# Performance work log

Measured on AMD Instinct MI355X. Metric: run time of the kernel, lower is better.

Reference implementation:

```python
import jax, jax.numpy as jnp
import numpy as np

EPS = 1e-5

def _ln(x, g, b):
    mu = jnp.mean(x, axis=-1, keepdims=True)
    var = jnp.var(x, axis=-1, keepdims=True)
    return (x - mu) * jax.lax.rsqrt(var + EPS) * g + b

def setup_inputs() -> dict:
    key = jax.random.key(0)
    ks = jax.random.split(key, 12)
    B, N, D, C = 1, 512, 128, 128
    s = 0.02
    return {
        "Z_raw": jax.random.normal(ks[0], (B, N, N, D), jnp.float32),
        "Z_mask_row": jnp.ones((B, N, N), jnp.float32),
        "ln1_g": jnp.ones((D,), jnp.float32),
        "ln1_b": jnp.zeros((D,), jnp.float32),
        "W_lr": jax.random.normal(ks[1], (D, 2 * C), jnp.float32) * s,
        "b_lr": jnp.zeros((2 * C,), jnp.float32),
        "W_gate": jax.random.normal(ks[2], (D, 2 * C), jnp.float32) * s,
        "b_gate": jnp.ones((2 * C,), jnp.float32),
        "W_og": jax.random.normal(ks[3], (D, D), jnp.float32) * s,
        "b_og": jnp.ones((D,), jnp.float32),
        "ln2_g": jnp.ones((C,), jnp.float32),
        "ln2_b": jnp.zeros((C,), jnp.float32),
        "W_op": jax.random.normal(ks[4], (C, D), jnp.float32) * s,
        "out_bias": jnp.zeros((D,), jnp.float32),
    }

def reference(Z_raw, Z_mask_row, ln1_g, ln1_b, W_lr, b_lr, W_gate, b_gate,
              W_og, b_og, ln2_g, ln2_b, W_op, out_bias):
    # Z_raw: [B,N,N,D]; Z_mask_row: [B,N,N]
    Z = _ln(Z_raw, ln1_g, ln1_b)
    lr = (Z @ W_lr + b_lr) * Z_mask_row[..., None]           # [B,N,N,2C]
    lr = lr * jax.nn.sigmoid(Z @ W_gate + b_gate)
    C = lr.shape[-1] // 2
    left, right = lr[..., :C], lr[..., C:]                    # [B,N,N,C]
    g = jax.nn.sigmoid(Z @ W_og + b_og)                       # [B,N,N,D]
    # triangle outgoing: p[b,i,j,c] = sum_k left[b,i,k,c] * right[b,j,k,c]
    p = jnp.einsum('bikc,bjkc->bijc', left, right)
    ab = _ln(p, ln2_g, ln2_b) @ W_op                          # [B,N,N,D]
    # eval mode: dropout mask is ones -> plain gated bias + residual
    return Z_raw + g * (ab + out_bias)
```

## Files before the change

kernel.cpp:

```cpp
#include <hip/hip_runtime.h>
#include <hip/hip_bf16.h>

#define NSEQ 512
#define DDIM 128
#define NPOS (NSEQ*NSEQ)

typedef __bf16 bf16x8 __attribute__((ext_vector_type(8)));
typedef float f32x4 __attribute__((ext_vector_type(4)));
typedef unsigned short us4 __attribute__((ext_vector_type(4)));
typedef unsigned int u32x4 __attribute__((ext_vector_type(4)));

__device__ __forceinline__ unsigned short f2bf(float f){
  unsigned int u = __float_as_uint(f);
  u += 0x7fffu + ((u >> 16) & 1u);
  return (unsigned short)(u >> 16);
}
__device__ __forceinline__ float bf2f(unsigned short s){
  return __uint_as_float(((unsigned int)s) << 16);
}
__device__ __forceinline__ float sigmoidf_(float x){
  return 1.0f/(1.0f + __expf(-x));
}

__global__ void k_prep(const float* __restrict__ Wlr, const float* __restrict__ Wgate,
                       const float* __restrict__ Wog, const float* __restrict__ Wop,
                       unsigned short* __restrict__ wt)
{
  int idx = blockIdx.x*256 + threadIdx.x;
  if (idx >= 768*128) return;
  int row = idx >> 7, k = idx & 127;
  float v;
  if (row < 256)      v = Wlr[k*256 + row];
  else if (row < 512) v = Wgate[k*256 + (row-256)];
  else if (row < 640) v = Wog[k*128 + (row-512)];
  else                v = Wop[k*128 + (row-640)];
  wt[idx] = f2bf(v);
}

__device__ __forceinline__ void mfma_k128(const unsigned short (&A)[128][136],
                                          const unsigned short (&B)[128][136],
                                          int wrow, int wcol, int lr_, int lq,
                                          f32x4 (&acc)[4][4])
{
  #pragma unroll
  for (int s = 0; s < 4; ++s){
    const int k0 = s*32 + lq*8;
    bf16x8 a[4], b[4];
    #pragma unroll
    for (int f = 0; f < 4; ++f)
      a[f] = *reinterpret_cast<const bf16x8*>(&A[wrow*64 + f*16 + lr_][k0]);
    #pragma unroll
    for (int f = 0; f < 4; ++f)
      b[f] = *reinterpret_cast<const bf16x8*>(&B[wcol*64 + f*16 + lr_][k0]);
    #pragma unroll
    for (int fi = 0; fi < 4; ++fi)
      #pragma unroll
      for (int fj = 0; fj < 4; ++fj)
        acc[fi][fj] = __builtin_amdgcn_mfma_f32_16x16x32_bf16(a[fi], b[fj], acc[fi][fj], 0, 0, 0);
  }
}

__global__ __launch_bounds__(256, 2)
void k1(const float* __restrict__ Zraw, const float* __restrict__ mask,
        const float* __restrict__ ln1g, const float* __restrict__ ln1b,
        const float* __restrict__ blr, const float* __restrict__ bgate,
        const float* __restrict__ bog,
        const unsigned short* __restrict__ wt,
        unsigned short* __restrict__ left_t, unsigned short* __restrict__ right_t,
        unsigned short* __restrict__ g_ws)
{
  __shared__ unsigned short zln[128][136];
  __shared__ unsigned short wchunk[128][136];

  const int t = threadIdx.x;
  const int posb = blockIdx.x * 128;
  const int r = t >> 1, h = t & 1;

  {
    const float* src = Zraw + (size_t)(posb + r)*DDIM + h*64;
    float v[64];
    float s = 0.f, sq = 0.f;
    #pragma unroll
    for (int i = 0; i < 16; ++i){
      f32x4 x = *reinterpret_cast<const f32x4*>(src + i*4);
      v[i*4+0] = x[0]; v[i*4+1] = x[1]; v[i*4+2] = x[2]; v[i*4+3] = x[3];
    }
    #pragma unroll
    for (int i = 0; i < 64; ++i){ s += v[i]; sq += v[i]*v[i]; }
    s  += __shfl_xor(s, 1);
    sq += __shfl_xor(sq, 1);
    float mu = s * (1.0f/128.0f);
    float var = sq * (1.0f/128.0f) - mu*mu;
    float rs = rsqrtf(var + 1e-5f);
    #pragma unroll
    for (int i = 0; i < 32; ++i){
      int c0 = h*64 + 2*i;
      float a = (v[2*i]   - mu)*rs*ln1g[c0]   + ln1b[c0];
      float b = (v[2*i+1] - mu)*rs*ln1g[c0+1] + ln1b[c0+1];
      *reinterpret_cast<unsigned int*>(&zln[r][c0]) =
          (unsigned int)f2bf(a) | ((unsigned int)f2bf(b) << 16);
    }
  }

  const int lane = t & 63;
  const int wid  = t >> 6;
  const int wrow = wid >> 1, wcol = wid & 1;
  const int lr_  = lane & 15, lq = lane >> 4;

  #pragma unroll 1
  for (int pair = 0; pair < 2; ++pair){
    __syncthreads();
    {
      const unsigned short* src = wt + (size_t)(256 + pair*128 + r)*128 + h*64;
      #pragma unroll
      for (int q = 0; q < 8; ++q)
        *reinterpret_cast<u32x4*>(&wchunk[r][h*64 + q*8]) =
            *reinterpret_cast<const u32x4*>(src + q*8);
    }
    __syncthreads();
    f32x4 accg[4][4];
    #pragma unroll
    for (int a1 = 0; a1 < 4; ++a1)
      #pragma unroll
      for (int a2 = 0; a2 < 4; ++a2) accg[a1][a2] = (f32x4){0.f,0.f,0.f,0.f};
    mfma_k128(zln, wchunk, wrow, wcol, lr_, lq, accg);

    float gsig[4][4][4];
    #pragma unroll
    for (int fi = 0; fi < 4; ++fi)
      #pragma unroll
      for (int fj = 0; fj < 4; ++fj){
        int col = wcol*64 + fj*16 + lr_;
        float bb = bgate[pair*128 + col];
        #pragma unroll
        for (int e = 0; e < 4; ++e)
          gsig[fi][fj][e] = sigmoidf_(accg[fi][fj][e] + bb);
      }

    __syncthreads();
    {
      const unsigned short* src = wt + (size_t)(pair*128 + r)*128 + h*64;
      #pragma unroll
      for (int q = 0; q < 8; ++q)
        *reinterpret_cast<u32x4*>(&wchunk[r][h*64 + q*8]) =
            *reinterpret_cast<const u32x4*>(src + q*8);
    }
    __syncthreads();
    f32x4 accl[4][4];
    #pragma unroll
    for (int a1 = 0; a1 < 4; ++a1)
      #pragma unroll
      for (int a2 = 0; a2 < 4; ++a2) accl[a1][a2] = (f32x4){0.f,0.f,0.f,0.f};
    mfma_k128(zln, wchunk, wrow, wcol, lr_, lq, accl);

    unsigned short* dst = pair ? right_t : left_t;
    #pragma unroll
    for (int fi = 0; fi < 4; ++fi){
      int rowb = wrow*64 + fi*16 + lq*4;
      float m0 = mask[posb + rowb + 0];
      float m1 = mask[posb + rowb + 1];
      float m2 = mask[posb + rowb + 2];
      float m3 = mask[posb + rowb + 3];
      #pragma unroll
      for (int fj = 0; fj < 4; ++fj){
        int col = wcol*64 + fj*16 + lr_;
        float bb = blr[pair*128 + col];
        us4 o;
        o[0] = f2bf((accl[fi][fj][0] + bb) * m0 * gsig[fi][fj][0]);
        o[1] = f2bf((accl[fi][fj][1] + bb) * m1 * gsig[fi][fj][1]);
        o[2] = f2bf((accl[fi][fj][2] + bb) * m2 * gsig[fi][fj][2]);
        o[3] = f2bf((accl[fi][fj][3] + bb) * m3 * gsig[fi][fj][3]);
        *reinterpret_cast<us4*>(dst + (size_t)col*NPOS + posb + rowb) = o;
      }
    }
  }

  __syncthreads();
  {
    const unsigned short* src = wt + (size_t)(512 + r)*128 + h*64;
    #pragma unroll
    for (int q = 0; q < 8; ++q)
      *reinterpret_cast<u32x4*>(&wchunk[r][h*64 + q*8]) =
          *reinterpret_cast<const u32x4*>(src + q*8);
  }
  __syncthreads();
  f32x4 acco[4][4];
  #pragma unroll
  for (int a1 = 0; a1 < 4; ++a1)
    #pragma unroll
    for (int a2 = 0; a2 < 4; ++a2) acco[a1][a2] = (f32x4){0.f,0.f,0.f,0.f};
  mfma_k128(zln, wchunk, wrow, wcol, lr_, lq, acco);
  __syncthreads();
  #pragma unroll
  for (int fi = 0; fi < 4; ++fi)
    #pragma unroll
    for (int fj = 0; fj < 4; ++fj){
      int col = wcol*64 + fj*16 + lr_;
      float bb = bog[col];
      #pragma unroll
      for (int e = 0; e < 4; ++e){
        int row = wrow*64 + fi*16 + lq*4 + e;
        zln[row][col] = f2bf(sigmoidf_(acco[fi][fj][e] + bb));
      }
    }
  __syncthreads();
  {
    unsigned short* dstg = g_ws + (size_t)(posb + r)*DDIM + h*64;
    #pragma unroll
    for (int q = 0; q < 8; ++q)
      *reinterpret_cast<u32x4*>(dstg + q*8) =
          *reinterpret_cast<const u32x4*>(&zln[r][h*64 + q*8]);
  }
}

__global__ __launch_bounds__(256, 3)
void k2(const unsigned short* __restrict__ left_t,
        const unsigned short* __restrict__ right_t,
        unsigned short* __restrict__ p_ws)
{
  __shared__ unsigned short At[128][72];
  __shared__ unsigned short Bt[128][72];

  const int t = threadIdx.x;
  const int c = blockIdx.y;
  const int it = blockIdx.x >> 2, jt = blockIdx.x & 3;
  const int i0 = it*128, j0 = jt*128;
  const int r = t >> 1, h = t & 1;
  const int lane = t & 63, wid = t >> 6;
  const int wrow = wid >> 1, wcol = wid & 1;
  const int lr_ = lane & 15, lq = lane >> 4;
  const size_t cbase = (size_t)c * NPOS;

  f32x4 acc[4][4];
  #pragma unroll
  for (int a1 = 0; a1 < 4; ++a1)
    #pragma unroll
    for (int a2 = 0; a2 < 4; ++a2) acc[a1][a2] = (f32x4){0.f,0.f,0.f,0.f};

  #pragma unroll 1
  for (int kk = 0; kk < 8; ++kk){
    const int k0 = kk*64;
    __syncthreads();
    {
      const unsigned short* sa = right_t + cbase + (size_t)(j0 + r)*NSEQ + k0 + h*32;
      const unsigned short* sb = left_t  + cbase + (size_t)(i0 + r)*NSEQ + k0 + h*32;
      #pragma unroll
      for (int q = 0; q < 4; ++q){
        *reinterpret_cast<u32x4*>(&At[r][h*32 + q*8]) = *reinterpret_cast<const u32x4*>(sa + q*8);
        *reinterpret_cast<u32x4*>(&Bt[r][h*32 + q*8]) = *reinterpret_cast<const u32x4*>(sb + q*8);
      }
    }
    __syncthreads();
    #pragma unroll
    for (int s = 0; s < 2; ++s){
      const int kl = s*32 + lq*8;
      bf16x8 a[4], b[4];
      #pragma unroll
      for (int f = 0; f < 4; ++f)
        a[f] = *reinterpret_cast<const bf16x8*>(&At[wrow*64 + f*16 + lr_][kl]);
      #pragma unroll
      for (int f = 0; f < 4; ++f)
        b[f] = *reinterpret_cast<const bf16x8*>(&Bt[wcol*64 + f*16 + lr_][kl]);
      #pragma unroll
      for (int fi = 0; fi < 4; ++fi)
        #pragma unroll
        for (int fj = 0; fj < 4; ++fj)
          acc[fi][fj] = __builtin_amdgcn_mfma_f32_16x16x32_bf16(a[fi], b[fj], acc[fi][fj], 0, 0, 0);
    }
  }

  #pragma unroll
  for (int fi = 0; fi < 4; ++fi){
    int jr = j0 + wrow*64 + fi*16 + lq*4;
    #pragma unroll
    for (int fj = 0; fj < 4; ++fj){
      int ic = i0 + wcol*64 + fj*16 + lr_;
      us4 o;
      o[0] = f2bf(acc[fi][fj][0]);
      o[1] = f2bf(acc[fi][fj][1]);
      o[2] = f2bf(acc[fi][fj][2]);
      o[3] = f2bf(acc[fi][fj][3]);
      *reinterpret_cast<us4*>(p_ws + cbase + (size_t)ic*NSEQ + jr) = o;
    }
  }
}

__global__ __launch_bounds__(256, 2)
void k3(const unsigned short* __restrict__ p_ws, const unsigned short* __restrict__ g_ws,
        const float* __restrict__ Zraw,
        const float* __restrict__ ln2g, const float* __restrict__ ln2b,
        const unsigned short* __restrict__ wt, const float* __restrict__ obias,
        float* __restrict__ out)
{
  __shared__ unsigned short pj[128][136];
  __shared__ unsigned short wop[128][136];
  __shared__ float part[8][32][8];
  __shared__ float mu_s[128], rs_s[128];

  const int t = threadIdx.x;
  const int i = blockIdx.x >> 2;
  const int j0 = (blockIdx.x & 3) * 128;
  const int r = t >> 1, h = t & 1;

  {
    const unsigned short* src = wt + (size_t)(640 + r)*128 + h*64;
    #pragma unroll
    for (int q = 0; q < 8; ++q)
      *reinterpret_cast<u32x4*>(&wop[r][h*64 + q*8]) =
          *reinterpret_cast<const u32x4*>(src + q*8);
  }

  {
    const int j4 = t & 31, grp = t >> 5;
    float s[4] = {0,0,0,0}, sq[4] = {0,0,0,0};
    const unsigned short* base = p_ws + (size_t)i*NSEQ + j0 + j4*4;
    #pragma unroll
    for (int it2 = 0; it2 < 16; ++it2){
      int c = grp + it2*8;
      us4 v = *reinterpret_cast<const us4*>(base + (size_t)c*NPOS);
      #pragma unroll
      for (int e = 0; e < 4; ++e){
        float f = bf2f(v[e]);
        s[e] += f; sq[e] += f*f;
      }
    }
    #pragma unroll
    for (int e = 0; e < 4; ++e){ part[grp][j4][e] = s[e]; part[grp][j4][4+e] = sq[e]; }
  }
  __syncthreads();
  if (t < 128){
    float s = 0.f, sq = 0.f;
    #pragma unroll
    for (int g2 = 0; g2 < 8; ++g2){
      s  += part[g2][t>>2][t&3];
      sq += part[g2][t>>2][4 + (t&3)];
    }
    float mu = s*(1.f/128.f);
    float var = sq*(1.f/128.f) - mu*mu;
    mu_s[t] = mu;
    rs_s[t] = rsqrtf(var + 1e-5f);
  }
  __syncthreads();

  {
    float mu = mu_s[r], rs = rs_s[r];
    const unsigned short* base = p_ws + (size_t)(h*64)*NPOS + (size_t)i*NSEQ + j0 + r;
    #pragma unroll
    for (int cc = 0; cc < 32; ++cc){
      int c0 = h*64 + 2*cc;
      float a = (bf2f(base[(size_t)(2*cc  )*NPOS]) - mu)*rs*ln2g[c0]   + ln2b[c0];
      float b = (bf2f(base[(size_t)(2*cc+1)*NPOS]) - mu)*rs*ln2g[c0+1] + ln2b[c0+1];
      *reinterpret_cast<unsigned int*>(&pj[r][c0]) =
          (unsigned int)f2bf(a) | ((unsigned int)f2bf(b) << 16);
    }
  }
  __syncthreads();

  const int lane = t & 63, wid = t >> 6;
  const int wrow = wid >> 1, wcol = wid & 1;
  const int lr_ = lane & 15, lq = lane >> 4;
  f32x4 acc[4][4];
  #pragma unroll
  for (int a1 = 0; a1 < 4; ++a1)
    #pragma unroll
    for (int a2 = 0; a2 < 4; ++a2) acc[a1][a2] = (f32x4){0.f,0.f,0.f,0.f};
  mfma_k128(pj, wop, wrow, wcol, lr_, lq, acc);

  #pragma unroll
  for (int fi = 0; fi < 4; ++fi){
    #pragma unroll
    for (int e = 0; e < 4; ++e){
      int jr = j0 + wrow*64 + fi*16 + lq*4 + e;
      size_t rowoff = ((size_t)i*NSEQ + jr)*DDIM;
      #pragma unroll
      for (int fj = 0; fj < 4; ++fj){
        int dd = wcol*64 + fj*16 + lr_;
        size_t off = rowoff + dd;
        float ab = acc[fi][fj][e] + obias[dd];
        out[off] = Zraw[off] + bf2f(g_ws[off]) * ab;
      }
    }
  }
}

extern "C" void kernel_launch(void* const* d_in, const int* in_sizes, int n_in,
                              void* d_out, int out_size, void* d_ws, size_t ws_size,
                              hipStream_t stream) {
  const float* Zraw  = (const float*)d_in[0];
  const float* mask  = (const float*)d_in[1];
  const float* ln1g  = (const float*)d_in[2];
  const float* ln1b  = (const float*)d_in[3];
  const float* Wlr   = (const float*)d_in[4];
  const float* blr   = (const float*)d_in[5];
  const float* Wgate = (const float*)d_in[6];
  const float* bgate = (const float*)d_in[7];
  const float* Wog   = (const float*)d_in[8];
  const float* bog   = (const float*)d_in[9];
  const float* ln2g  = (const float*)d_in[10];
  const float* ln2b  = (const float*)d_in[11];
  const float* Wop   = (const float*)d_in[12];
  const float* obias = (const float*)d_in[13];
  float* out = (float*)d_out;

  unsigned short* wt      = (unsigned short*)d_ws;
  unsigned short* left_t  = wt + 768*128;
  unsigned short* right_t = left_t + (size_t)DDIM*NPOS;
  unsigned short* g_ws    = right_t + (size_t)DDIM*NPOS;
  unsigned short* p_ws    = g_ws + (size_t)DDIM*NPOS;

  k_prep<<<384, 256, 0, stream>>>(Wlr, Wgate, Wog, Wop, wt);
  k1<<<NPOS/128, 256, 0, stream>>>(Zraw, mask, ln1g, ln1b, blr, bgate, bog,
                                   wt, left_t, right_t, g_ws);
  k2<<<dim3(16, 128), 256, 0, stream>>>(left_t, right_t, p_ws);
  k3<<<NPOS/128, 256, 0, stream>>>(p_ws, g_ws, Zraw, ln2g, ln2b, wt, obias, out);
}
```

Measured before the change: 549.4 us.

## Restructure k1 to read weights from global, enlarge k2 tiles, reuse p loads in k3

k1 drops the shared weight staging buffer. Each warp now owns 32 rows and reads the bf16 weight fragments straight from global/L2 in 64-column halves, which cuts shared memory and syncs and allows higher occupancy. k2 moves to 256x256 tiles with 512 threads to raise reuse of left/right per load. k3 caches the p values in shared memory during the statistics pass, so LayerNorm no longer reloads them with strided global reads. The costs are more global weight traffic in k1, higher register pressure in k2, and k2 running only 512 blocks.

```diff
diff --git a/kernel.cpp b/kernel.cpp
--- a/kernel.cpp
+++ b/kernel.cpp
@@ -37,30 +37,29 @@
   wt[idx] = f2bf(v);
 }
 
-__device__ __forceinline__ void mfma_k128(const unsigned short (&A)[128][136],
-                                          const unsigned short (&B)[128][136],
-                                          int wrow, int wcol, int lr_, int lq,
-                                          f32x4 (&acc)[4][4])
+__device__ __forceinline__ void gemm64(const unsigned short (&A)[128][136],
+                                       const unsigned short* __restrict__ wbase,
+                                       int wid, int lr_, int lq, f32x4 (&acc)[2][4])
 {
   #pragma unroll
   for (int s = 0; s < 4; ++s){
     const int k0 = s*32 + lq*8;
-    bf16x8 a[4], b[4];
-    #pragma unroll
-    for (int f = 0; f < 4; ++f)
-      a[f] = *reinterpret_cast<const bf16x8*>(&A[wrow*64 + f*16 + lr_][k0]);
-    #pragma unroll
-    for (int f = 0; f < 4; ++f)
-      b[f] = *reinterpret_cast<const bf16x8*>(&B[wcol*64 + f*16 + lr_][k0]);
-    #pragma unroll
-    for (int fi = 0; fi < 4; ++fi)
+    bf16x8 a[2], b[4];
+    #pragma unroll
+    for (int fi = 0; fi < 2; ++fi)
+      a[fi] = *reinterpret_cast<const bf16x8*>(&A[wid*32 + fi*16 + lr_][k0]);
+    #pragma unroll
+    for (int fj = 0; fj < 4; ++fj)
+      b[fj] = *reinterpret_cast<const bf16x8*>(wbase + ((fj*16 + lr_) << 7) + k0);
+    #pragma unroll
+    for (int fi = 0; fi < 2; ++fi)
       #pragma unroll
       for (int fj = 0; fj < 4; ++fj)
         acc[fi][fj] = __builtin_amdgcn_mfma_f32_16x16x32_bf16(a[fi], b[fj], acc[fi][fj], 0, 0, 0);
   }
 }
 
-__global__ __launch_bounds__(256, 2)
+__global__ __launch_bounds__(256, 4)
 void k1(const float* __restrict__ Zraw, const float* __restrict__ mask,
         const float* __restrict__ ln1g, const float* __restrict__ ln1b,
         const float* __restrict__ blr, const float* __restrict__ bgate,
@@ -70,11 +69,12 @@
         unsigned short* __restrict__ g_ws)
 {
   __shared__ unsigned short zln[128][136];
-  __shared__ unsigned short wchunk[128][136];
 
   const int t = threadIdx.x;
   const int posb = blockIdx.x * 128;
   const int r = t >> 1, h = t & 1;
+  const int lane = t & 63, wid = t >> 6;
+  const int lr_ = lane & 15, lq = lane >> 4;
 
   {
     const float* src = Zraw + (size_t)(posb + r)*DDIM + h*64;
@@ -93,116 +93,95 @@
     float var = sq * (1.0f/128.0f) - mu*mu;
     float rs = rsqrtf(var + 1e-5f);
     #pragma unroll
-    for (int i = 0; i < 32; ++i){
-      int c0 = h*64 + 2*i;
-      float a = (v[2*i]   - mu)*rs*ln1g[c0]   + ln1b[c0];
-      float b = (v[2*i+1] - mu)*rs*ln1g[c0+1] + ln1b[c0+1];
-      *reinterpret_cast<unsigned int*>(&zln[r][c0]) =
-          (unsigned int)f2bf(a) | ((unsigned int)f2bf(b) << 16);
-    }
-  }
-
-  const int lane = t & 63;
-  const int wid  = t >> 6;
-  const int wrow = wid >> 1, wcol = wid & 1;
-  const int lr_  = lane & 15, lq = lane >> 4;
+    for (int q = 0; q < 8; ++q){
+      u32x4 pk;
+      #pragma unroll
+      for (int e = 0; e < 4; ++e){
+        int c0 = h*64 + q*8 + 2*e;
+        float a = (v[q*8+2*e]   - mu)*rs*ln1g[c0]   + ln1b[c0];
+        float b = (v[q*8+2*e+1] - mu)*rs*ln1g[c0+1] + ln1b[c0+1];
+        pk[e] = (unsigned int)f2bf(a) | ((unsigned int)f2bf(b) << 16);
+      }
+      *reinterpret_cast<u32x4*>(&zln[r][h*64 + q*8]) = pk;
+    }
+  }
+  __syncthreads();
+
+  float mpre[2][4];
+  #pragma unroll
+  for (int fi = 0; fi < 2; ++fi)
+    #pragma unroll
+    for (int e = 0; e < 4; ++e)
+      mpre[fi][e] = mask[posb + wid*32 + fi*16 + lq*4 + e];
 
   #pragma unroll 1
   for (int pair = 0; pair < 2; ++pair){
-    __syncthreads();
-    {
-      const unsigned short* src = wt + (size_t)(256 + pair*128 + r)*128 + h*64;
-      #pragma unroll
-      for (int q = 0; q < 8; ++q)
-        *reinterpret_cast<u32x4*>(&wchunk[r][h*64 + q*8]) =
-            *reinterpret_cast<const u32x4*>(src + q*8);
-    }
-    __syncthreads();
-    f32x4 accg[4][4];
-    #pragma unroll
-    for (int a1 = 0; a1 < 4; ++a1)
-      #pragma unroll
-      for (int a2 = 0; a2 < 4; ++a2) accg[a1][a2] = (f32x4){0.f,0.f,0.f,0.f};
-    mfma_k128(zln, wchunk, wrow, wcol, lr_, lq, accg);
-
-    float gsig[4][4][4];
-    #pragma unroll
-    for (int fi = 0; fi < 4; ++fi)
+    unsigned short* dst = pair ? right_t : left_t;
+    #pragma unroll 1
+    for (int half = 0; half < 2; ++half){
+      const int colb = half*64;
+      f32x4 ag[2][4];
+      #pragma unroll
+      for (int a1 = 0; a1 < 2; ++a1)
+        #pragma unroll
+        for (int a2 = 0; a2 < 4; ++a2) ag[a1][a2] = (f32x4){0.f,0.f,0.f,0.f};
+      gemm64(zln, wt + (size_t)(256 + pair*128 + colb)*128, wid, lr_, lq, ag);
+      float gs[2][4][4];
+      #pragma unroll
+      for (int fi = 0; fi < 2; ++fi)
+        #pragma unroll
+        for (int fj = 0; fj < 4; ++fj){
+          float bb = bgate[pair*128 + colb + fj*16 + lr_];
+          #pragma unroll
+          for (int e = 0; e < 4; ++e)
+            gs[fi][fj][e] = sigmoidf_(ag[fi][fj][e] + bb);
+        }
+      f32x4 al[2][4];
+      #pragma unroll
+      for (int a1 = 0; a1 < 2; ++a1)
+        #pragma unroll
+        for (int a2 = 0; a2 < 4; ++a2) al[a1][a2] = (f32x4){0.f,0.f,0.f,0.f};
+      gemm64(zln, wt + (size_t)(pair*128 + colb)*128, wid, lr_, lq, al);
+      #pragma unroll
+      for (int fi = 0; fi < 2; ++fi){
+        const int rowb = wid*32 + fi*16 + lq*4;
+        #pragma unroll
+        for (int fj = 0; fj < 4; ++fj){
+          const int col = colb + fj*16 + lr_;
+          float bb = blr[pair*128 + col];
+          us4 o;
+          o[0] = f2bf((al[fi][fj][0] + bb) * mpre[fi][0] * gs[fi][fj][0]);
+          o[1] = f2bf((al[fi][fj][1] + bb) * mpre[fi][1] * gs[fi][fj][1]);
+          o[2] = f2bf((al[fi][fj][2] + bb) * mpre[fi][2] * gs[fi][fj][2]);
+          o[3] = f2bf((al[fi][fj][3] + bb) * mpre[fi][3] * gs[fi][fj][3]);
+          *reinterpret_cast<us4*>(dst + (size_t)col*NPOS + posb + rowb) = o;
+        }
+      }
+    }
+  }
+
+  f32x4 ao[2][2][4];
+  #pragma unroll
+  for (int hf = 0; hf < 2; ++hf){
+    #pragma unroll
+    for (int a1 = 0; a1 < 2; ++a1)
+      #pragma unroll
+      for (int a2 = 0; a2 < 4; ++a2) ao[hf][a1][a2] = (f32x4){0.f,0.f,0.f,0.f};
+    gemm64(zln, wt + (size_t)(512 + hf*64)*128, wid, lr_, lq, ao[hf]);
+  }
+  __syncthreads();
+  #pragma unroll
+  for (int hf = 0; hf < 2; ++hf)
+    #pragma unroll
+    for (int fi = 0; fi < 2; ++fi)
       #pragma unroll
       for (int fj = 0; fj < 4; ++fj){
-        int col = wcol*64 + fj*16 + lr_;
-        float bb = bgate[pair*128 + col];
+        const int col = hf*64 + fj*16 + lr_;
+        float bb = bog[col];
         #pragma unroll
         for (int e = 0; e < 4; ++e)
-          gsig[fi][fj][e] = sigmoidf_(accg[fi][fj][e] + bb);
-      }
-
-    __syncthreads();
-    {
-      const unsigned short* src = wt + (size_t)(pair*128 + r)*128 + h*64;
-      #pragma unroll
-      for (int q = 0; q < 8; ++q)
-        *reinterpret_cast<u32x4*>(&wchunk[r][h*64 + q*8]) =
-            *reinterpret_cast<const u32x4*>(src + q*8);
-    }
-    __syncthreads();
-    f32x4 accl[4][4];
-    #pragma unroll
-    for (int a1 = 0; a1 < 4; ++a1)
-      #pragma unroll
-      for (int a2 = 0; a2 < 4; ++a2) accl[a1][a2] = (f32x4){0.f,0.f,0.f,0.f};
-    mfma_k128(zln, wchunk, wrow, wcol, lr_, lq, accl);
-
-    unsigned short* dst = pair ? right_t : left_t;
-    #pragma unroll
-    for (int fi = 0; fi < 4; ++fi){
-      int rowb = wrow*64 + fi*16 + lq*4;
-      float m0 = mask[posb + rowb + 0];
-      float m1 = mask[posb + rowb + 1];
-      float m2 = mask[posb + rowb + 2];
-      float m3 = mask[posb + rowb + 3];
-      #pragma unroll
-      for (int fj = 0; fj < 4; ++fj){
-        int col = wcol*64 + fj*16 + lr_;
-        float bb = blr[pair*128 + col];
-        us4 o;
-        o[0] = f2bf((accl[fi][fj][0] + bb) * m0 * gsig[fi][fj][0]);
-        o[1] = f2bf((accl[fi][fj][1] + bb) * m1 * gsig[fi][fj][1]);
-        o[2] = f2bf((accl[fi][fj][2] + bb) * m2 * gsig[fi][fj][2]);
-        o[3] = f2bf((accl[fi][fj][3] + bb) * m3 * gsig[fi][fj][3]);
-        *reinterpret_cast<us4*>(dst + (size_t)col*NPOS + posb + rowb) = o;
-      }
-    }
-  }
-
-  __syncthreads();
-  {
-    const unsigned short* src = wt + (size_t)(512 + r)*128 + h*64;
-    #pragma unroll
-    for (int q = 0; q < 8; ++q)
-      *reinterpret_cast<u32x4*>(&wchunk[r][h*64 + q*8]) =
-          *reinterpret_cast<const u32x4*>(src + q*8);
-  }
-  __syncthreads();
-  f32x4 acco[4][4];
-  #pragma unroll
-  for (int a1 = 0; a1 < 4; ++a1)
-    #pragma unroll
-    for (int a2 = 0; a2 < 4; ++a2) acco[a1][a2] = (f32x4){0.f,0.f,0.f,0.f};
-  mfma_k128(zln, wchunk, wrow, wcol, lr_, lq, acco);
-  __syncthreads();
-  #pragma unroll
-  for (int fi = 0; fi < 4; ++fi)
-    #pragma unroll
-    for (int fj = 0; fj < 4; ++fj){
-      int col = wcol*64 + fj*16 + lr_;
-      float bb = bog[col];
-      #pragma unroll
-      for (int e = 0; e < 4; ++e){
-        int row = wrow*64 + fi*16 + lq*4 + e;
-        zln[row][col] = f2bf(sigmoidf_(acco[fi][fj][e] + bb));
-      }
-    }
+          zln[wid*32 + fi*16 + lq*4 + e][col] = f2bf(sigmoidf_(ao[hf][fi][fj][e] + bb));
+      }
   __syncthreads();
   {
     unsigned short* dstg = g_ws + (size_t)(posb + r)*DDIM + h*64;
@@ -213,27 +192,28 @@
   }
 }
 
-__global__ __launch_bounds__(256, 3)
+__global__ __launch_bounds__(512, 1)
 void k2(const unsigned short* __restrict__ left_t,
         const unsigned short* __restrict__ right_t,
         unsigned short* __restrict__ p_ws)
 {
-  __shared__ unsigned short At[128][72];
-  __shared__ unsigned short Bt[128][72];
+  __shared__ unsigned short At[256][72];
+  __shared__ unsigned short Bt[256][72];
 
   const int t = threadIdx.x;
   const int c = blockIdx.y;
-  const int it = blockIdx.x >> 2, jt = blockIdx.x & 3;
-  const int i0 = it*128, j0 = jt*128;
-  const int r = t >> 1, h = t & 1;
+  const int it = blockIdx.x >> 1, jt = blockIdx.x & 1;
+  const int i0 = it*256, j0 = jt*256;
   const int lane = t & 63, wid = t >> 6;
-  const int wrow = wid >> 1, wcol = wid & 1;
+  const int wr = wid >> 2, wc = wid & 3;
   const int lr_ = lane & 15, lq = lane >> 4;
   const size_t cbase = (size_t)c * NPOS;
-
-  f32x4 acc[4][4];
-  #pragma unroll
-  for (int a1 = 0; a1 < 4; ++a1)
+  const int rs_ = t >> 3;
+  const int cs_ = (t & 7) * 8;
+
+  f32x4 acc[8][4];
+  #pragma unroll
+  for (int a1 = 0; a1 < 8; ++a1)
     #pragma unroll
     for (int a2 = 0; a2 < 4; ++a2) acc[a1][a2] = (f32x4){0.f,0.f,0.f,0.f};
 
@@ -241,28 +221,27 @@
   for (int kk = 0; kk < 8; ++kk){
     const int k0 = kk*64;
     __syncthreads();
-    {
-      const unsigned short* sa = right_t + cbase + (size_t)(j0 + r)*NSEQ + k0 + h*32;
-      const unsigned short* sb = left_t  + cbase + (size_t)(i0 + r)*NSEQ + k0 + h*32;
-      #pragma unroll
-      for (int q = 0; q < 4; ++q){
-        *reinterpret_cast<u32x4*>(&At[r][h*32 + q*8]) = *reinterpret_cast<const u32x4*>(sa + q*8);
-        *reinterpret_cast<u32x4*>(&Bt[r][h*32 + q*8]) = *reinterpret_cast<const u32x4*>(sb + q*8);
-      }
+    #pragma unroll
+    for (int q = 0; q < 4; ++q){
+      const int rr = q*64 + rs_;
+      *reinterpret_cast<u32x4*>(&At[rr][cs_]) =
+          *reinterpret_cast<const u32x4*>(right_t + cbase + (size_t)(j0+rr)*NSEQ + k0 + cs_);
+      *reinterpret_cast<u32x4*>(&Bt[rr][cs_]) =
+          *reinterpret_cast<const u32x4*>(left_t  + cbase + (size_t)(i0+rr)*NSEQ + k0 + cs_);
     }
     __syncthreads();
     #pragma unroll
     for (int s = 0; s < 2; ++s){
       const int kl = s*32 + lq*8;
-      bf16x8 a[4], b[4];
+      bf16x8 a[8], b[4];
+      #pragma unroll
+      for (int f = 0; f < 8; ++f)
+        a[f] = *reinterpret_cast<const bf16x8*>(&At[wr*128 + f*16 + lr_][kl]);
       #pragma unroll
       for (int f = 0; f < 4; ++f)
-        a[f] = *reinterpret_cast<const bf16x8*>(&At[wrow*64 + f*16 + lr_][kl]);
-      #pragma unroll
-      for (int f = 0; f < 4; ++f)
-        b[f] = *reinterpret_cast<const bf16x8*>(&Bt[wcol*64 + f*16 + lr_][kl]);
-      #pragma unroll
-      for (int fi = 0; fi < 4; ++fi)
+        b[f] = *reinterpret_cast<const bf16x8*>(&Bt[wc*64 + f*16 + lr_][kl]);
+      #pragma unroll
+      for (int fi = 0; fi < 8; ++fi)
         #pragma unroll
         for (int fj = 0; fj < 4; ++fj)
           acc[fi][fj] = __builtin_amdgcn_mfma_f32_16x16x32_bf16(a[fi], b[fj], acc[fi][fj], 0, 0, 0);
@@ -270,11 +249,11 @@
   }
 
   #pragma unroll
-  for (int fi = 0; fi < 4; ++fi){
-    int jr = j0 + wrow*64 + fi*16 + lq*4;
+  for (int fi = 0; fi < 8; ++fi){
+    const int jr = j0 + wr*128 + fi*16 + lq*4;
     #pragma unroll
     for (int fj = 0; fj < 4; ++fj){
-      int ic = i0 + wcol*64 + fj*16 + lr_;
+      const int ic = i0 + wc*64 + fj*16 + lr_;
       us4 o;
       o[0] = f2bf(acc[fi][fj][0]);
       o[1] = f2bf(acc[fi][fj][1]);
@@ -285,6 +264,29 @@
   }
 }
 
+__device__ __forceinline__ void mfma_k128(const unsigned short (&A)[128][136],
+                                          const unsigned short (&B)[128][136],
+                                          int wrow, int wcol, int lr_, int lq,
+                                          f32x4 (&acc)[4][4])
+{
+  #pragma unroll
+  for (int s = 0; s < 4; ++s){
+    const int k0 = s*32 + lq*8;
+    bf16x8 a[4], b[4];
+    #pragma unroll
+    for (int f = 0; f < 4; ++f)
+      a[f] = *reinterpret_cast<const bf16x8*>(&A[wrow*64 + f*16 + lr_][k0]);
+    #pragma unroll
+    for (int f = 0; f < 4; ++f)
+      b[f] = *reinterpret_cast<const bf16x8*>(&B[wcol*64 + f*16 + lr_][k0]);
+    #pragma unroll
+    for (int fi = 0; fi < 4; ++fi)
+      #pragma unroll
+      for (int fj = 0; fj < 4; ++fj)
+        acc[fi][fj] = __builtin_amdgcn_mfma_f32_16x16x32_bf16(a[fi], b[fj], acc[fi][fj], 0, 0, 0);
+  }
+}
+
 __global__ __launch_bounds__(256, 2)
 void k3(const unsigned short* __restrict__ p_ws, const unsigned short* __restrict__ g_ws,
         const float* __restrict__ Zraw,
@@ -316,12 +318,13 @@
     const unsigned short* base = p_ws + (size_t)i*NSEQ + j0 + j4*4;
     #pragma unroll
     for (int it2 = 0; it2 < 16; ++it2){
-      int c = grp + it2*8;
-      us4 v = *reinterpret_cast<const us4*>(base + (size_t)c*NPOS);
+      int cc = grp + it2*8;
+      us4 v = *reinterpret_cast<const us4*>(base + (size_t)cc*NPOS);
       #pragma unroll
       for (int e = 0; e < 4; ++e){
         float f = bf2f(v[e]);
         s[e] += f; sq[e] += f*f;
+        pj[j4*4 + e][cc] = v[e];
       }
     }
     #pragma unroll
@@ -344,14 +347,20 @@
 
   {
     float mu = mu_s[r], rs = rs_s[r];
-    const unsigned short* base = p_ws + (size_t)(h*64)*NPOS + (size_t)i*NSEQ + j0 + r;
-    #pragma unroll
-    for (int cc = 0; cc < 32; ++cc){
-      int c0 = h*64 + 2*cc;
-      float a = (bf2f(base[(size_t)(2*cc  )*NPOS]) - mu)*rs*ln2g[c0]   + ln2b[c0];
-      float b = (bf2f(base[(size_t)(2*cc+1)*NPOS]) - mu)*rs*ln2g[c0+1] + ln2b[c0+1];
-      *reinterpret_cast<unsigned int*>(&pj[r][c0]) =
-          (unsigned int)f2bf(a) | ((unsigned int)f2bf(b) << 16);
+    #pragma unroll
+    for (int q = 0; q < 8; ++q){
+      const int c0 = h*64 + q*8;
+      u32x4 pk = *reinterpret_cast<const u32x4*>(&pj[r][c0]);
+      u32x4 o;
+      #pragma unroll
+      for (int e = 0; e < 4; ++e){
+        const int cc = c0 + 2*e;
+        unsigned int w2 = pk[e];
+        float a = (bf2f((unsigned short)(w2 & 0xffffu)) - mu)*rs*ln2g[cc]   + ln2b[cc];
+        float b = (bf2f((unsigned short)(w2 >> 16))     - mu)*rs*ln2g[cc+1] + ln2b[cc+1];
+        o[e] = (unsigned int)f2bf(a) | ((unsigned int)f2bf(b) << 16);
+      }
+      *reinterpret_cast<u32x4*>(&pj[r][c0]) = o;
     }
   }
   __syncthreads();
@@ -370,12 +379,12 @@
   for (int fi = 0; fi < 4; ++fi){
     #pragma unroll
     for (int e = 0; e < 4; ++e){
-      int jr = j0 + wrow*64 + fi*16 + lq*4 + e;
-      size_t rowoff = ((size_t)i*NSEQ + jr)*DDIM;
+      const int jr = j0 + wrow*64 + fi*16 + lq*4 + e;
+      const size_t rowoff = ((size_t)i*NSEQ + jr)*DDIM;
       #pragma unroll
       for (int fj = 0; fj < 4; ++fj){
-        int dd = wcol*64 + fj*16 + lr_;
-        size_t off = rowoff + dd;
+        const int dd = wcol*64 + fj*16 + lr_;
+        const size_t off = rowoff + dd;
         float ab = acc[fi][fj][e] + obias[dd];
         out[off] = Zraw[off] + bf2f(g_ws[off]) * ab;
       }
@@ -411,6 +420,6 @@
   k_prep<<<384, 256, 0, stream>>>(Wlr, Wgate, Wog, Wop, wt);
   k1<<<NPOS/128, 256, 0, stream>>>(Zraw, mask, ln1g, ln1b, blr, bgate, bog,
                                    wt, left_t, right_t, g_ws);
-  k2<<<dim3(16, 128), 256, 0, stream>>>(left_t, right_t, p_ws);
+  k2<<<dim3(4, 128), 512, 0, stream>>>(left_t, right_t, p_ws);
   k3<<<NPOS/128, 256, 0, stream>>>(p_ws, g_ws, Zraw, ln2g, ln2b, wt, obias, out);
 }
```

Measured after the change: 626.3 us. 1.14x slower.
